# Performance work log

Hardware: AMD Instinct MI355X
Metric: run time of the kernel (lower is better)

The kernel has to match this reference:

```python
import jax, jax.numpy as jnp
import numpy as np

B, S, D, H = 2, 2048, 1024, 16
DH = D // H  # 64

def setup_inputs() -> dict:
    key = jax.random.key(0)
    ks = jax.random.split(key, 7)
    scale = 1.0 / np.sqrt(DH)
    return {
        "seqs": jax.random.normal(ks[0], (B, S, D), dtype=jnp.float32),
        "Wq": jax.random.normal(ks[1], (H, DH, DH), dtype=jnp.float32) * scale,
        "bq": jax.random.normal(ks[2], (H, DH), dtype=jnp.float32) * scale,
        "Wk": jax.random.normal(ks[3], (H, DH, DH), dtype=jnp.float32) * scale,
        "bk": jax.random.normal(ks[4], (H, DH), dtype=jnp.float32) * scale,
        "Wv": jax.random.normal(ks[5], (H, DH, DH), dtype=jnp.float32) * scale,
        "bv": jax.random.normal(ks[6], (H, DH), dtype=jnp.float32) * scale,
    }

def reference(seqs, Wq, bq, Wk, bk, Wv, bv):
    b, s, d = seqs.shape
    h, dh = Wq.shape[0], Wq.shape[1]
    x = seqs.reshape(b, s, h, dh)  # per-head slice of d_model
    # torch Linear: y = x @ W.T + b ; W[h] is [out, in]
    q = jnp.einsum('bshd,hed->bshe', x, Wq) + bq
    k = jnp.einsum('bshd,hed->bshe', x, Wk) + bk
    v = jnp.einsum('bshd,hed->bshe', x, Wv) + bv
    inv_sqrt = 1.0 / (dh ** 0.5)
    scores = jnp.einsum('bqhd,bkhd->bhqk', q, k) * inv_sqrt  # [B,H,S,S]
    attn = jax.nn.softmax(scores, axis=-1)
    out = jnp.einsum('bhqk,bkhd->bqhd', attn, v)  # [B,S,H,DH]
    return out.reshape(b, s, d)
```

## Files before the change

### kernel.cpp

```cpp
#include <hip/hip_runtime.h>
#include <hip/hip_bf16.h>
#include <cmath>

#define BB 2
#define SS 2048
#define DD 1024
#define HH 16
#define DHH 64
#define NT (SS / 64)
#define QBLK 128

typedef __bf16 v8bf __attribute__((ext_vector_type(8)));
typedef float f32x4 __attribute__((ext_vector_type(4)));

static __device__ __forceinline__ __bf16 f2bf(float f) {
    __hip_bfloat16 h = __float2bfloat16(f);
    return __builtin_bit_cast(__bf16, h);
}
static __device__ __forceinline__ unsigned pk2(float a, float b) {
    unsigned short ua = __builtin_bit_cast(unsigned short, f2bf(a));
    unsigned short ub = __builtin_bit_cast(unsigned short, f2bf(b));
    return (unsigned)ua | ((unsigned)ub << 16);
}

#define SCQ 0.1803368801111204f

__global__ __launch_bounds__(256) void qkv_kernel(
    const float* __restrict__ seqs,
    const float* __restrict__ Wq, const float* __restrict__ bq,
    const float* __restrict__ Wk, const float* __restrict__ bk,
    const float* __restrict__ Wv, const float* __restrict__ bv,
    __bf16* __restrict__ q_ws, __bf16* __restrict__ k_ws,
    __bf16* __restrict__ vt_ws)
{
    const int h  = blockIdx.y;
    const int b  = blockIdx.x / (SS / 64);
    const int st = blockIdx.x % (SS / 64);
    const int s0 = st * 64;
    const int tid  = threadIdx.x;
    const int lane = tid & 63;
    const int w    = tid >> 6;
    const int lr   = lane & 15;
    const int lg   = lane >> 4;

    __shared__ __bf16 x_lds[64][72];
    __shared__ __bf16 w_lds[3][64][72];
    __shared__ __bf16 v_lds[64][72];

#pragma unroll
    for (int i = 0; i < 4; ++i) {
        int idx = tid + i * 256;
        int r   = idx >> 4;
        int c4  = (idx & 15) * 4;
        float4 v = *reinterpret_cast<const float4*>(
            &seqs[((size_t)b * SS + s0 + r) * DD + h * DHH + c4]);
        uint2 u;
        u.x = pk2(v.x, v.y);
        u.y = pk2(v.z, v.w);
        *reinterpret_cast<uint2*>(&x_lds[r][c4]) = u;
    }
    const float* Wsrc[3] = { Wq + (size_t)h * DHH * DHH,
                             Wk + (size_t)h * DHH * DHH,
                             Wv + (size_t)h * DHH * DHH };
#pragma unroll
    for (int m = 0; m < 3; ++m) {
        const float ws_ = (m == 0) ? SCQ : 1.0f;
#pragma unroll
        for (int i = 0; i < 4; ++i) {
            int idx = tid + i * 256;
            int r   = idx >> 4;
            int c4  = (idx & 15) * 4;
            float4 v = *reinterpret_cast<const float4*>(&Wsrc[m][r * DHH + c4]);
            uint2 u;
            u.x = pk2(v.x * ws_, v.y * ws_);
            u.y = pk2(v.z * ws_, v.w * ws_);
            *reinterpret_cast<uint2*>(&w_lds[m][r][c4]) = u;
        }
    }
    __syncthreads();

    v8bf a0 = *reinterpret_cast<const v8bf*>(&x_lds[w * 16 + lr][lg * 8]);
    v8bf a1 = *reinterpret_cast<const v8bf*>(&x_lds[w * 16 + lr][32 + lg * 8]);

#pragma unroll
    for (int m = 0; m < 2; ++m) {
        const float* bias = (m == 0) ? bq + h * DHH : bk + h * DHH;
        const float bsc   = (m == 0) ? SCQ : 1.0f;
        __bf16* dst = (m == 0) ? q_ws : k_ws;
#pragma unroll
        for (int cg = 0; cg < 4; ++cg) {
            v8bf b0 = *reinterpret_cast<const v8bf*>(&w_lds[m][cg * 16 + lr][lg * 8]);
            v8bf b1 = *reinterpret_cast<const v8bf*>(&w_lds[m][cg * 16 + lr][32 + lg * 8]);
            f32x4 acc = {0.f, 0.f, 0.f, 0.f};
            acc = __builtin_amdgcn_mfma_f32_16x16x32_bf16(b0, a0, acc, 0, 0, 0);
            acc = __builtin_amdgcn_mfma_f32_16x16x32_bf16(b1, a1, acc, 0, 0, 0);
            const int e0 = cg * 16 + lg * 4;
            uint2 u;
            u.x = pk2(acc[0] + bias[e0 + 0] * bsc, acc[1] + bias[e0 + 1] * bsc);
            u.y = pk2(acc[2] + bias[e0 + 2] * bsc, acc[3] + bias[e0 + 3] * bsc);
            *reinterpret_cast<uint2*>(
                &dst[(((size_t)b * HH + h) * SS + s0 + w * 16 + lr) * DHH + e0]) = u;
        }
    }

    {
        const float* bias = bv + h * DHH;
#pragma unroll
        for (int cg = 0; cg < 4; ++cg) {
            v8bf b0 = *reinterpret_cast<const v8bf*>(&w_lds[2][cg * 16 + lr][lg * 8]);
            v8bf b1 = *reinterpret_cast<const v8bf*>(&w_lds[2][cg * 16 + lr][32 + lg * 8]);
            f32x4 acc = {0.f, 0.f, 0.f, 0.f};
            acc = __builtin_amdgcn_mfma_f32_16x16x32_bf16(a0, b0, acc, 0, 0, 0);
            acc = __builtin_amdgcn_mfma_f32_16x16x32_bf16(a1, b1, acc, 0, 0, 0);
            const int   e   = cg * 16 + lr;
            const float bb_ = bias[e];
            uint2 u;
            u.x = pk2(acc[0] + bb_, acc[1] + bb_);
            u.y = pk2(acc[2] + bb_, acc[3] + bb_);
            *reinterpret_cast<uint2*>(&v_lds[e][w * 16 + lg * 4]) = u;
        }
    }
    __syncthreads();

#pragma unroll
    for (int i = 0; i < 2; ++i) {
        int idx = tid + i * 256;
        int e   = idx >> 3;
        int c8  = (idx & 7) * 8;
        uint4 v = *reinterpret_cast<const uint4*>(&v_lds[e][c8]);
        *reinterpret_cast<uint4*>(
            &vt_ws[(((size_t)b * HH + h) * DHH + e) * SS + s0 + c8]) = v;
    }
}

__global__ __launch_bounds__(512) void flash_kernel(
    const __bf16* __restrict__ q_ws, const __bf16* __restrict__ k_ws,
    const __bf16* __restrict__ vt_ws, float* __restrict__ out)
{
    const int bh = blockIdx.y;
    const int b  = bh / HH;
    const int h  = bh % HH;
    const int s0 = blockIdx.x * QBLK;
    const int tid  = threadIdx.x;
    const int lane = tid & 63;
    const int w    = tid >> 6;
    const int lr   = lane & 15;
    const int lg   = lane >> 4;

    __shared__ __bf16 kv_lds[2][2][64 * 64];
    __shared__ __bf16 p_lds[QBLK][72];

    const size_t qbase = ((size_t)bh * SS + s0) * DHH;
    v8bf qa0 = *reinterpret_cast<const v8bf*>(&q_ws[qbase + (w * 16 + lr) * DHH + lg * 8]);
    v8bf qa1 = *reinterpret_cast<const v8bf*>(&q_ws[qbase + (w * 16 + lr) * DHH + 32 + lg * 8]);

    const __bf16* kg = k_ws  + (size_t)bh * SS * DHH;
    const __bf16* vg = vt_ws + (size_t)bh * DHH * SS;

    f32x4 acc[4];
#pragma unroll
    for (int cg = 0; cg < 4; ++cg) acc[cg] = (f32x4){0.f, 0.f, 0.f, 0.f};
    float m_run = -INFINITY;
    float l_run = 0.f;

    const int srow = lane >> 3;
    const int scol = 8 * ((lane & 7) ^ srow);

    auto stage = [&](int buf, int kt) {
        const __bf16* srck = kg + (size_t)(kt * 64 + w * 8 + srow) * DHH + scol;
        __builtin_amdgcn_global_load_lds(
            (const __attribute__((address_space(1))) unsigned int*)srck,
            (__attribute__((address_space(3))) unsigned int*)&kv_lds[buf][0][w * 512],
            16, 0, 0);
        const __bf16* srcv = vg + (size_t)(w * 8 + srow) * SS + kt * 64 + scol;
        __builtin_amdgcn_global_load_lds(
            (const __attribute__((address_space(1))) unsigned int*)srcv,
            (__attribute__((address_space(3))) unsigned int*)&kv_lds[buf][1][w * 512],
            16, 0, 0);
    };

    stage(0, 0);
    __syncthreads();

    int cur = 0;
    for (int kt = 0; kt < NT; ++kt) {
        if (kt + 1 < NT) stage(cur ^ 1, kt + 1);

        const __bf16* kb = &kv_lds[cur][0][0];
        const __bf16* vb = &kv_lds[cur][1][0];
        const int sw = (lr & 7);

        f32x4 sc[4];
        __builtin_amdgcn_s_setprio(1);
#pragma unroll
        for (int cg = 0; cg < 4; ++cg) {
            int row = cg * 16 + lr;
            v8bf a0 = *reinterpret_cast<const v8bf*>(&kb[row * 64 + 8 * (lg ^ sw)]);
            v8bf a1 = *reinterpret_cast<const v8bf*>(&kb[row * 64 + 8 * ((4 + lg) ^ sw)]);
            f32x4 t = {0.f, 0.f, 0.f, 0.f};
            t = __builtin_amdgcn_mfma_f32_16x16x32_bf16(a0, qa0, t, 0, 0, 0);
            t = __builtin_amdgcn_mfma_f32_16x16x32_bf16(a1, qa1, t, 0, 0, 0);
            sc[cg] = t;
        }
        __builtin_amdgcn_s_setprio(0);

        float mloc = sc[0][0];
#pragma unroll
        for (int cg = 0; cg < 4; ++cg)
#pragma unroll
            for (int r = 0; r < 4; ++r) mloc = fmaxf(mloc, sc[cg][r]);
        mloc = fmaxf(mloc, __shfl_xor(mloc, 16));
        mloc = fmaxf(mloc, __shfl_xor(mloc, 32));

        if (__any(mloc > m_run + 8.0f)) {
            float m_new = fmaxf(m_run, mloc);
            float corr  = exp2f(m_run - m_new);
            m_run = m_new;
            l_run *= corr;
            float cb[4];
#pragma unroll
            for (int r = 0; r < 4; ++r) cb[r] = __shfl(corr, lg * 4 + r);
#pragma unroll
            for (int cg = 0; cg < 4; ++cg)
#pragma unroll
                for (int r = 0; r < 4; ++r) acc[cg][r] *= cb[r];
        }

        float rs = 0.f;
#pragma unroll
        for (int cg = 0; cg < 4; ++cg) {
            float p0 = exp2f(sc[cg][0] - m_run);
            float p1 = exp2f(sc[cg][1] - m_run);
            float p2 = exp2f(sc[cg][2] - m_run);
            float p3 = exp2f(sc[cg][3] - m_run);
            rs += (p0 + p1) + (p2 + p3);
            uint2 u;
            u.x = pk2(p0, p1);
            u.y = pk2(p2, p3);
            *reinterpret_cast<uint2*>(&p_lds[w * 16 + lr][cg * 16 + lg * 4]) = u;
        }
        rs += __shfl_xor(rs, 16);
        rs += __shfl_xor(rs, 32);
        l_run += rs;

        v8bf pa0 = *reinterpret_cast<const v8bf*>(&p_lds[w * 16 + lr][lg * 8]);
        v8bf pa1 = *reinterpret_cast<const v8bf*>(&p_lds[w * 16 + lr][32 + lg * 8]);
        __builtin_amdgcn_s_setprio(1);
#pragma unroll
        for (int cg = 0; cg < 4; ++cg) {
            int row = cg * 16 + lr;
            v8bf b0 = *reinterpret_cast<const v8bf*>(&vb[row * 64 + 8 * (lg ^ sw)]);
            v8bf b1 = *reinterpret_cast<const v8bf*>(&vb[row * 64 + 8 * ((4 + lg) ^ sw)]);
            acc[cg] = __builtin_amdgcn_mfma_f32_16x16x32_bf16(pa0, b0, acc[cg], 0, 0, 0);
            acc[cg] = __builtin_amdgcn_mfma_f32_16x16x32_bf16(pa1, b1, acc[cg], 0, 0, 0);
        }
        __builtin_amdgcn_s_setprio(0);

        __syncthreads();
        cur ^= 1;
    }

    float linv[4];
#pragma unroll
    for (int r = 0; r < 4; ++r) linv[r] = 1.0f / __shfl(l_run, lg * 4 + r);
#pragma unroll
    for (int cg = 0; cg < 4; ++cg)
#pragma unroll
        for (int r = 0; r < 4; ++r) {
            int sr = s0 + w * 16 + lg * 4 + r;
            int e  = cg * 16 + lr;
            out[((size_t)b * SS + sr) * DD + h * DHH + e] = acc[cg][r] * linv[r];
        }
}

extern "C" void kernel_launch(void* const* d_in, const int* in_sizes, int n_in,
                              void* d_out, int out_size, void* d_ws, size_t ws_size,
                              hipStream_t stream)
{
    const float* seqs = (const float*)d_in[0];
    const float* Wq   = (const float*)d_in[1];
    const float* bq   = (const float*)d_in[2];
    const float* Wk   = (const float*)d_in[3];
    const float* bk   = (const float*)d_in[4];
    const float* Wv   = (const float*)d_in[5];
    const float* bv   = (const float*)d_in[6];
    float* out = (float*)d_out;

    const size_t per = (size_t)BB * HH * SS * DHH;
    __bf16* q_ws  = (__bf16*)d_ws;
    __bf16* k_ws  = q_ws + per;
    __bf16* vt_ws = k_ws + per;

    dim3 gridp(BB * (SS / 64), HH);
    qkv_kernel<<<gridp, 256, 0, stream>>>(seqs, Wq, bq, Wk, bk, Wv, bv,
                                          q_ws, k_ws, vt_ws);
    dim3 gridf(SS / QBLK, BB * HH);
    flash_kernel<<<gridf, 512, 0, stream>>>(q_ws, k_ws, vt_ws, out);
}
```

Baseline: 156.9 us.

## Split KV tiles across wave pairs in flash kernel and pre-convert weights

The flash kernel now uses 64-query blocks, each handled by 8 waves arranged as 4 query groups by 2 KV halves. Each wave computes scores for half of every 64-key tile, and the two partial softmax states are merged through LDS at the end. This doubles the grid to give more blocks for occupancy, at the cost of a final combine step and reduced per-wave MFMA work. A separate small kernel converts the weights and biases to bf16 once, so qkv_kernel reads them from global memory instead of converting per block into LDS. That adds an extra launch.

```diff
diff --git a/kernel.cpp b/kernel.cpp
--- a/kernel.cpp
+++ b/kernel.cpp
@@ -8,7 +8,6 @@
 #define HH 16
 #define DHH 64
 #define NT (SS / 64)
-#define QBLK 128
 
 typedef __bf16 v8bf __attribute__((ext_vector_type(8)));
 typedef float f32x4 __attribute__((ext_vector_type(4)));
@@ -25,11 +24,39 @@
 
 #define SCQ 0.1803368801111204f
 
-__global__ __launch_bounds__(256) void qkv_kernel(
-    const float* __restrict__ seqs,
+__global__ __launch_bounds__(256) void wconv_kernel(
     const float* __restrict__ Wq, const float* __restrict__ bq,
     const float* __restrict__ Wk, const float* __restrict__ bk,
     const float* __restrict__ Wv, const float* __restrict__ bv,
+    __bf16* __restrict__ wb, float* __restrict__ bb)
+{
+    const int tid = threadIdx.x;
+    if (blockIdx.x < 192) {
+        int idx = blockIdx.x * 1024 + tid * 4;
+        int m   = idx >> 16;
+        int rem = idx & 65535;
+        const float* src = (m == 0) ? Wq : (m == 1) ? Wk : Wv;
+        float4 v = *reinterpret_cast<const float4*>(&src[rem]);
+        float s  = (m == 0) ? SCQ : 1.0f;
+        uint2 u;
+        u.x = pk2(v.x * s, v.y * s);
+        u.y = pk2(v.z * s, v.w * s);
+        *reinterpret_cast<uint2*>(&wb[idx]) = u;
+    } else {
+#pragma unroll
+        for (int j = 0; j < 12; ++j) {
+            int idx = j * 256 + tid;
+            int m   = idx >> 10;
+            int rem = idx & 1023;
+            const float* src = (m == 0) ? bq : (m == 1) ? bk : bv;
+            bb[idx] = src[rem] * ((m == 0) ? SCQ : 1.0f);
+        }
+    }
+}
+
+__global__ __launch_bounds__(256) void qkv_kernel(
+    const float* __restrict__ seqs,
+    const __bf16* __restrict__ wb, const float* __restrict__ bb,
     __bf16* __restrict__ q_ws, __bf16* __restrict__ k_ws,
     __bf16* __restrict__ vt_ws)
 {
@@ -44,7 +71,6 @@
     const int lg   = lane >> 4;
 
     __shared__ __bf16 x_lds[64][72];
-    __shared__ __bf16 w_lds[3][64][72];
     __shared__ __bf16 v_lds[64][72];
 
 #pragma unroll
@@ -59,24 +85,6 @@
         u.y = pk2(v.z, v.w);
         *reinterpret_cast<uint2*>(&x_lds[r][c4]) = u;
     }
-    const float* Wsrc[3] = { Wq + (size_t)h * DHH * DHH,
-                             Wk + (size_t)h * DHH * DHH,
-                             Wv + (size_t)h * DHH * DHH };
-#pragma unroll
-    for (int m = 0; m < 3; ++m) {
-        const float ws_ = (m == 0) ? SCQ : 1.0f;
-#pragma unroll
-        for (int i = 0; i < 4; ++i) {
-            int idx = tid + i * 256;
-            int r   = idx >> 4;
-            int c4  = (idx & 15) * 4;
-            float4 v = *reinterpret_cast<const float4*>(&Wsrc[m][r * DHH + c4]);
-            uint2 u;
-            u.x = pk2(v.x * ws_, v.y * ws_);
-            u.y = pk2(v.z * ws_, v.w * ws_);
-            *reinterpret_cast<uint2*>(&w_lds[m][r][c4]) = u;
-        }
-    }
     __syncthreads();
 
     v8bf a0 = *reinterpret_cast<const v8bf*>(&x_lds[w * 16 + lr][lg * 8]);
@@ -84,36 +92,38 @@
 
 #pragma unroll
     for (int m = 0; m < 2; ++m) {
-        const float* bias = (m == 0) ? bq + h * DHH : bk + h * DHH;
-        const float bsc   = (m == 0) ? SCQ : 1.0f;
+        const __bf16* wm = wb + ((size_t)m * HH + h) * DHH * DHH;
+        const float*  bm = bb + ((size_t)m * HH + h) * DHH;
         __bf16* dst = (m == 0) ? q_ws : k_ws;
 #pragma unroll
         for (int cg = 0; cg < 4; ++cg) {
-            v8bf b0 = *reinterpret_cast<const v8bf*>(&w_lds[m][cg * 16 + lr][lg * 8]);
-            v8bf b1 = *reinterpret_cast<const v8bf*>(&w_lds[m][cg * 16 + lr][32 + lg * 8]);
+            v8bf b0 = *reinterpret_cast<const v8bf*>(&wm[(cg * 16 + lr) * DHH + lg * 8]);
+            v8bf b1 = *reinterpret_cast<const v8bf*>(&wm[(cg * 16 + lr) * DHH + 32 + lg * 8]);
             f32x4 acc = {0.f, 0.f, 0.f, 0.f};
             acc = __builtin_amdgcn_mfma_f32_16x16x32_bf16(b0, a0, acc, 0, 0, 0);
             acc = __builtin_amdgcn_mfma_f32_16x16x32_bf16(b1, a1, acc, 0, 0, 0);
             const int e0 = cg * 16 + lg * 4;
+            float4 bi = *reinterpret_cast<const float4*>(&bm[e0]);
             uint2 u;
-            u.x = pk2(acc[0] + bias[e0 + 0] * bsc, acc[1] + bias[e0 + 1] * bsc);
-            u.y = pk2(acc[2] + bias[e0 + 2] * bsc, acc[3] + bias[e0 + 3] * bsc);
+            u.x = pk2(acc[0] + bi.x, acc[1] + bi.y);
+            u.y = pk2(acc[2] + bi.z, acc[3] + bi.w);
             *reinterpret_cast<uint2*>(
                 &dst[(((size_t)b * HH + h) * SS + s0 + w * 16 + lr) * DHH + e0]) = u;
         }
     }
 
     {
-        const float* bias = bv + h * DHH;
+        const __bf16* wm = wb + ((size_t)2 * HH + h) * DHH * DHH;
+        const float*  bm = bb + ((size_t)2 * HH + h) * DHH;
 #pragma unroll
         for (int cg = 0; cg < 4; ++cg) {
-            v8bf b0 = *reinterpret_cast<const v8bf*>(&w_lds[2][cg * 16 + lr][lg * 8]);
-            v8bf b1 = *reinterpret_cast<const v8bf*>(&w_lds[2][cg * 16 + lr][32 + lg * 8]);
+            v8bf b0 = *reinterpret_cast<const v8bf*>(&wm[(cg * 16 + lr) * DHH + lg * 8]);
+            v8bf b1 = *reinterpret_cast<const v8bf*>(&wm[(cg * 16 + lr) * DHH + 32 + lg * 8]);
             f32x4 acc = {0.f, 0.f, 0.f, 0.f};
             acc = __builtin_amdgcn_mfma_f32_16x16x32_bf16(a0, b0, acc, 0, 0, 0);
             acc = __builtin_amdgcn_mfma_f32_16x16x32_bf16(a1, b1, acc, 0, 0, 0);
             const int   e   = cg * 16 + lr;
-            const float bb_ = bias[e];
+            const float bb_ = bm[e];
             uint2 u;
             u.x = pk2(acc[0] + bb_, acc[1] + bb_);
             u.y = pk2(acc[2] + bb_, acc[3] + bb_);
@@ -140,19 +150,22 @@
     const int bh = blockIdx.y;
     const int b  = bh / HH;
     const int h  = bh % HH;
-    const int s0 = blockIdx.x * QBLK;
+    const int s0 = blockIdx.x * 64;
     const int tid  = threadIdx.x;
     const int lane = tid & 63;
     const int w    = tid >> 6;
+    const int wq   = w >> 1;
+    const int wk   = w & 1;
     const int lr   = lane & 15;
     const int lg   = lane >> 4;
 
     __shared__ __bf16 kv_lds[2][2][64 * 64];
-    __shared__ __bf16 p_lds[QBLK][72];
+    __shared__ __bf16 p_lds[64][72];
+    __shared__ float  ml_lds[2][64];
 
     const size_t qbase = ((size_t)bh * SS + s0) * DHH;
-    v8bf qa0 = *reinterpret_cast<const v8bf*>(&q_ws[qbase + (w * 16 + lr) * DHH + lg * 8]);
-    v8bf qa1 = *reinterpret_cast<const v8bf*>(&q_ws[qbase + (w * 16 + lr) * DHH + 32 + lg * 8]);
+    v8bf qa0 = *reinterpret_cast<const v8bf*>(&q_ws[qbase + (wq * 16 + lr) * DHH + lg * 8]);
+    v8bf qa1 = *reinterpret_cast<const v8bf*>(&q_ws[qbase + (wq * 16 + lr) * DHH + 32 + lg * 8]);
 
     const __bf16* kg = k_ws  + (size_t)bh * SS * DHH;
     const __bf16* vg = vt_ws + (size_t)bh * DHH * SS;
@@ -165,6 +178,7 @@
 
     const int srow = lane >> 3;
     const int scol = 8 * ((lane & 7) ^ srow);
+    const int sw   = lr & 7;
 
     auto stage = [&](int buf, int kt) {
         const __bf16* srck = kg + (size_t)(kt * 64 + w * 8 + srow) * DHH + scol;
@@ -188,13 +202,12 @@
 
         const __bf16* kb = &kv_lds[cur][0][0];
         const __bf16* vb = &kv_lds[cur][1][0];
-        const int sw = (lr & 7);
-
-        f32x4 sc[4];
+
+        f32x4 sc[2];
         __builtin_amdgcn_s_setprio(1);
 #pragma unroll
-        for (int cg = 0; cg < 4; ++cg) {
-            int row = cg * 16 + lr;
+        for (int cg = 0; cg < 2; ++cg) {
+            int row = wk * 32 + cg * 16 + lr;
             v8bf a0 = *reinterpret_cast<const v8bf*>(&kb[row * 64 + 8 * (lg ^ sw)]);
             v8bf a1 = *reinterpret_cast<const v8bf*>(&kb[row * 64 + 8 * ((4 + lg) ^ sw)]);
             f32x4 t = {0.f, 0.f, 0.f, 0.f};
@@ -206,7 +219,7 @@
 
         float mloc = sc[0][0];
 #pragma unroll
-        for (int cg = 0; cg < 4; ++cg)
+        for (int cg = 0; cg < 2; ++cg)
 #pragma unroll
             for (int r = 0; r < 4; ++r) mloc = fmaxf(mloc, sc[cg][r]);
         mloc = fmaxf(mloc, __shfl_xor(mloc, 16));
@@ -226,33 +239,27 @@
                 for (int r = 0; r < 4; ++r) acc[cg][r] *= cb[r];
         }
 
-        float rs = 0.f;
-#pragma unroll
-        for (int cg = 0; cg < 4; ++cg) {
+#pragma unroll
+        for (int cg = 0; cg < 2; ++cg) {
             float p0 = exp2f(sc[cg][0] - m_run);
             float p1 = exp2f(sc[cg][1] - m_run);
             float p2 = exp2f(sc[cg][2] - m_run);
             float p3 = exp2f(sc[cg][3] - m_run);
-            rs += (p0 + p1) + (p2 + p3);
+            l_run += (p0 + p1) + (p2 + p3);
             uint2 u;
             u.x = pk2(p0, p1);
             u.y = pk2(p2, p3);
-            *reinterpret_cast<uint2*>(&p_lds[w * 16 + lr][cg * 16 + lg * 4]) = u;
-        }
-        rs += __shfl_xor(rs, 16);
-        rs += __shfl_xor(rs, 32);
-        l_run += rs;
-
-        v8bf pa0 = *reinterpret_cast<const v8bf*>(&p_lds[w * 16 + lr][lg * 8]);
-        v8bf pa1 = *reinterpret_cast<const v8bf*>(&p_lds[w * 16 + lr][32 + lg * 8]);
+            *reinterpret_cast<uint2*>(
+                &p_lds[wq * 16 + lr][wk * 32 + cg * 16 + lg * 4]) = u;
+        }
+
+        v8bf pa = *reinterpret_cast<const v8bf*>(&p_lds[wq * 16 + lr][wk * 32 + lg * 8]);
         __builtin_amdgcn_s_setprio(1);
 #pragma unroll
         for (int cg = 0; cg < 4; ++cg) {
             int row = cg * 16 + lr;
-            v8bf b0 = *reinterpret_cast<const v8bf*>(&vb[row * 64 + 8 * (lg ^ sw)]);
-            v8bf b1 = *reinterpret_cast<const v8bf*>(&vb[row * 64 + 8 * ((4 + lg) ^ sw)]);
-            acc[cg] = __builtin_amdgcn_mfma_f32_16x16x32_bf16(pa0, b0, acc[cg], 0, 0, 0);
-            acc[cg] = __builtin_amdgcn_mfma_f32_16x16x32_bf16(pa1, b1, acc[cg], 0, 0, 0);
+            v8bf vb0 = *reinterpret_cast<const v8bf*>(&vb[row * 64 + 8 * ((wk * 4 + lg) ^ sw)]);
+            acc[cg] = __builtin_amdgcn_mfma_f32_16x16x32_bf16(pa, vb0, acc[cg], 0, 0, 0);
         }
         __builtin_amdgcn_s_setprio(0);
 
@@ -260,17 +267,48 @@
         cur ^= 1;
     }
 
-    float linv[4];
-#pragma unroll
-    for (int r = 0; r < 4; ++r) linv[r] = 1.0f / __shfl(l_run, lg * 4 + r);
-#pragma unroll
-    for (int cg = 0; cg < 4; ++cg)
+    float l_row = l_run + __shfl_xor(l_run, 16);
+    l_row += __shfl_xor(l_row, 32);
+
+    float* comb = reinterpret_cast<float*>(&kv_lds[0][0][0]);
+    if (wk == 1) {
+        if (lg == 0) {
+            ml_lds[0][wq * 16 + lr] = m_run;
+            ml_lds[1][wq * 16 + lr] = l_row;
+        }
+#pragma unroll
+        for (int cg = 0; cg < 4; ++cg)
+#pragma unroll
+            for (int r = 0; r < 4; ++r)
+                comb[(wq * 16 + lg * 4 + r) * 64 + cg * 16 + lr] = acc[cg][r];
+    }
+    __syncthreads();
+    if (wk == 0) {
+        float m_b = ml_lds[0][wq * 16 + lr];
+        float l_b = ml_lds[1][wq * 16 + lr];
+        float m12 = fmaxf(m_run, m_b);
+        float ca  = exp2f(m_run - m12);
+        float cbf = exp2f(m_b - m12);
+        float inv = 1.0f / (l_row * ca + l_b * cbf);
+        float caR[4], cbR[4], li[4];
 #pragma unroll
         for (int r = 0; r < 4; ++r) {
-            int sr = s0 + w * 16 + lg * 4 + r;
-            int e  = cg * 16 + lr;
-            out[((size_t)b * SS + sr) * DD + h * DHH + e] = acc[cg][r] * linv[r];
-        }
+            int src = lg * 4 + r;
+            caR[r] = __shfl(ca, src);
+            cbR[r] = __shfl(cbf, src);
+            li[r]  = __shfl(inv, src);
+        }
+#pragma unroll
+        for (int cg = 0; cg < 4; ++cg)
+#pragma unroll
+            for (int r = 0; r < 4; ++r) {
+                float ob = comb[(wq * 16 + lg * 4 + r) * 64 + cg * 16 + lr];
+                float o  = (acc[cg][r] * caR[r] + ob * cbR[r]) * li[r];
+                int sr = s0 + wq * 16 + lg * 4 + r;
+                int e  = cg * 16 + lr;
+                out[((size_t)b * SS + sr) * DD + h * DHH + e] = o;
+            }
+    }
 }
 
 extern "C" void kernel_launch(void* const* d_in, const int* in_sizes, int n_in,
@@ -290,10 +328,14 @@
     __bf16* q_ws  = (__bf16*)d_ws;
     __bf16* k_ws  = q_ws + per;
     __bf16* vt_ws = k_ws + per;
+    __bf16* wb    = vt_ws + per;
+    float*  bb    = (float*)(wb + 3 * HH * DHH * DHH);
+
+    wconv_kernel<<<193, 256, 0, stream>>>(Wq, bq, Wk, bk, Wv, bv, wb, bb);
 
     dim3 gridp(BB * (SS / 64), HH);
-    qkv_kernel<<<gridp, 256, 0, stream>>>(seqs, Wq, bq, Wk, bk, Wv, bv,
-                                          q_ws, k_ws, vt_ws);
-    dim3 gridf(SS / QBLK, BB * HH);
+    qkv_kernel<<<gridp, 256, 0, stream>>>(seqs, wb, bb, q_ws, k_ws, vt_ws);
+
+    dim3 gridf(SS / 64, BB * HH);
     flash_kernel<<<gridf, 512, 0, stream>>>(q_ws, k_ws, vt_ws, out);
 }
```

New measurement: 173.6 us. 10.7% more time.
